# Performance work log

Measured on AMD Instinct MI355X. Metric: run time of the kernel, lower is better.

Reference implementation:

```python
import jax, jax.numpy as jnp
import numpy as np

N_NODES = 100000
N_EDGES = 1600000
HID = 64
EDGE_DIM = 16
SC_DIM = 6  # max_cycle(8) - MIN_CYCLE(3) + 1
N_LAYERS = 2
MSG_IN = 2 * HID + 2 * SC_DIM + EDGE_DIM  # 156
UPD_IN = 2 * HID


def setup_inputs() -> dict:
    key = jax.random.key(0)
    ks = jax.random.split(key, 16)
    s = 0.05
    inp = {
        "x": jax.random.normal(ks[0], (N_NODES, HID), dtype=jnp.float32),
        "edge_list": jax.random.randint(ks[1], (N_EDGES, 2), 0, N_NODES, dtype=jnp.int32),
        "node_struct": jax.random.randint(ks[2], (N_NODES, SC_DIM), 0, 4, dtype=jnp.int32),
        "edge_feature": jax.random.normal(ks[3], (N_EDGES, EDGE_DIM), dtype=jnp.float32),
        "edge_weight": jnp.ones((N_EDGES,), dtype=jnp.float32),
        "node2graph": jnp.sort(jax.random.randint(ks[4], (N_NODES,), 0, 128, dtype=jnp.int32)),
        "num_graphs": 128,
        # params
        "lin_w": jax.random.normal(ks[5], (HID, HID), dtype=jnp.float32) * s,
        "lin_b": jnp.zeros((HID,), dtype=jnp.float32),
        "msg_w1": jax.random.normal(ks[6], (N_LAYERS, MSG_IN, HID), dtype=jnp.float32) * s,
        "msg_b1": jnp.zeros((N_LAYERS, HID), dtype=jnp.float32),
        "msg_w2": jax.random.normal(ks[7], (N_LAYERS, HID, HID), dtype=jnp.float32) * s,
        "msg_b2": jnp.zeros((N_LAYERS, HID), dtype=jnp.float32),
        "upd_w1": jax.random.normal(ks[8], (N_LAYERS, UPD_IN, HID), dtype=jnp.float32) * s,
        "upd_b1": jnp.zeros((N_LAYERS, HID), dtype=jnp.float32),
        "upd_w2": jax.random.normal(ks[9], (N_LAYERS, HID, HID), dtype=jnp.float32) * s,
        "upd_b2": jnp.zeros((N_LAYERS, HID), dtype=jnp.float32),
    }
    return inp


def reference(x, edge_list, node_struct, edge_feature, edge_weight, node2graph,
              num_graphs, lin_w, lin_b, msg_w1, msg_b1, msg_w2, msg_b2,
              upd_w1, upd_b1, upd_w2, upd_b2):
    n_node = x.shape[0]
    src = edge_list[:, 0]
    dst = edge_list[:, 1]
    sc = node_struct.astype(x.dtype)          # [N, 6] structural cycle counts
    h = x @ lin_w + lin_b                      # input projection [N, HID]
    for l in range(N_LAYERS):
        # message: gather endpoints + structural feats + edge feats, 2-layer MLP
        m = jnp.concatenate([h[src], h[dst], sc[src], sc[dst], edge_feature], axis=-1)
        m = jax.nn.relu(m @ msg_w1[l] + msg_b1[l]) @ msg_w2[l] + msg_b2[l]
        # aggregate: weighted scatter_add onto destination nodes
        upd = jax.ops.segment_sum(m * edge_weight[:, None], dst, num_segments=n_node)
        # combine: cat(input, update) -> 2-layer MLP -> outer activation
        z = jnp.concatenate([h, upd], axis=-1)
        z = jax.nn.relu(z @ upd_w1[l] + upd_b1[l]) @ upd_w2[l] + upd_b2[l]
        h = jax.nn.relu(z)
    node_feature = h
    graph_feature = jax.ops.segment_sum(node_feature, node2graph, num_segments=num_graphs)
    return graph_feature, node_feature
```

## Files before the change

### kernel.cpp

```cpp
#include <hip/hip_runtime.h>

#define NN 100000
#define NE 1600000
#define HID 64
#define MSG_IN 156
#define W1E_OFF 140

__device__ __forceinline__ void mm4x4(float (&acc)[4][4], const float4 a, const float4 b) {
    acc[0][0] = fmaf(a.x, b.x, acc[0][0]);
    acc[0][1] = fmaf(a.x, b.y, acc[0][1]);
    acc[0][2] = fmaf(a.x, b.z, acc[0][2]);
    acc[0][3] = fmaf(a.x, b.w, acc[0][3]);
    acc[1][0] = fmaf(a.y, b.x, acc[1][0]);
    acc[1][1] = fmaf(a.y, b.y, acc[1][1]);
    acc[1][2] = fmaf(a.y, b.z, acc[1][2]);
    acc[1][3] = fmaf(a.y, b.w, acc[1][3]);
    acc[2][0] = fmaf(a.z, b.x, acc[2][0]);
    acc[2][1] = fmaf(a.z, b.y, acc[2][1]);
    acc[2][2] = fmaf(a.z, b.z, acc[2][2]);
    acc[2][3] = fmaf(a.z, b.w, acc[2][3]);
    acc[3][0] = fmaf(a.w, b.x, acc[3][0]);
    acc[3][1] = fmaf(a.w, b.y, acc[3][1]);
    acc[3][2] = fmaf(a.w, b.z, acc[3][2]);
    acc[3][3] = fmaf(a.w, b.w, acc[3][3]);
}


__global__ __launch_bounds__(256) void k_sw(
    const int2* __restrict__ el2, const float* __restrict__ ew,
    float* __restrict__ sw, int n_edges)
{
    int e = blockIdx.x * 256 + threadIdx.x;
    if (e < n_edges) atomicAdd(&sw[el2[e].y], ew[e]);
}

__global__ __launch_bounds__(256) void k_hist(
    const int2* __restrict__ el2, int* __restrict__ counts, int n_edges)
{
    int e = blockIdx.x * 256 + threadIdx.x;
    if (e < n_edges) atomicAdd(&counts[el2[e].y], 1);
}

__global__ __launch_bounds__(256) void k_scan1(
    const int* counts, int* offs, int* __restrict__ blksum, int n)
{
    __shared__ int s[256];
    const int tid = threadIdx.x;
    int i = blockIdx.x * 256 + tid;
    int v = (i < n) ? counts[i] : 0;
    s[tid] = v;
    for (int off = 1; off < 256; off <<= 1) {
        __syncthreads();
        int t = (tid >= off) ? s[tid - off] : 0;
        __syncthreads();
        s[tid] += t;
    }
    __syncthreads();
    if (i < n) offs[i] = s[tid] - v;
    if (tid == 255) blksum[blockIdx.x] = s[255];
}

__global__ __launch_bounds__(512) void k_scan2(int* __restrict__ blksum, int nb)
{
    __shared__ int s[512];
    const int tid = threadIdx.x;
    int v = (tid < nb) ? blksum[tid] : 0;
    s[tid] = v;
    for (int off = 1; off < 512; off <<= 1) {
        __syncthreads();
        int t = (tid >= off) ? s[tid - off] : 0;
        __syncthreads();
        s[tid] += t;
    }
    __syncthreads();
    if (tid < nb) blksum[tid] = s[tid] - v;
}

__global__ __launch_bounds__(256) void k_scan3(
    int* __restrict__ offs, const int* __restrict__ blksum, int n)
{
    int i = blockIdx.x * 256 + threadIdx.x;
    if (i < n) offs[i] += blksum[blockIdx.x];
}

__global__ __launch_bounds__(256) void k_permute(
    const int2* __restrict__ el2, int* __restrict__ cursor,
    int* __restrict__ perm, int n_edges)
{
    int e = blockIdx.x * 256 + threadIdx.x;
    if (e < n_edges) {
        int pos = atomicAdd(&cursor[el2[e].y], 1);
        perm[pos] = e;
    }
}

__global__ __launch_bounds__(256) void k_csmall(
    const float* __restrict__ msg_w2, const float* __restrict__ upd_w1,
    const float* __restrict__ msg_b2, float* __restrict__ C2, float* __restrict__ db2)
{
    const int l = blockIdx.x;
    const float* W2  = msg_w2 + (size_t)l * 4096;
    const float* U1b = upd_w1 + (size_t)l * 8192 + 4096;
    const float* b2  = msg_b2 + l * 64;
    float* C  = C2  + (size_t)l * 4096;
    float* db = db2 + l * 64;
    __shared__ __align__(16) float At[64][68];
    __shared__ __align__(16) float B[64][64];
    const int tid = threadIdx.x;
    for (int i = tid; i < 1024; i += 256) {
        ((float4*)B)[i] = ((const float4*)U1b)[i];
        int m = i >> 4, f4 = i & 15, k4 = f4 * 4;
        float4 v = ((const float4*)W2)[m * 16 + f4];
        At[k4 + 0][m] = v.x; At[k4 + 1][m] = v.y; At[k4 + 2][m] = v.z; At[k4 + 3][m] = v.w;
    }
    __syncthreads();
    const int ty = tid >> 4, tx = tid & 15;
    float acc[4][4];
    #pragma unroll
    for (int r = 0; r < 4; ++r) { acc[r][0]=0.f; acc[r][1]=0.f; acc[r][2]=0.f; acc[r][3]=0.f; }
    #pragma unroll 8
    for (int k = 0; k < 64; ++k) {
        float4 a = *(const float4*)&At[k][ty * 4];
        float4 bv = *(const float4*)&B[k][tx * 4];
        mm4x4(acc, a, bv);
    }
    #pragma unroll
    for (int r = 0; r < 4; ++r)
        ((float4*)C)[(ty * 4 + r) * 16 + tx] = make_float4(acc[r][0], acc[r][1], acc[r][2], acc[r][3]);
    if (tid < 64) {
        float sum = 0.f;
        for (int k = 0; k < 64; ++k) sum += b2[k] * B[k][tid];
        db[tid] = sum;
    }
}


__global__ __launch_bounds__(256) void k_init(
    const float* __restrict__ x, const float* __restrict__ w,
    const float* __restrict__ b, float* __restrict__ h, int n)
{
    __shared__ __align__(16) float At[64][68];
    __shared__ __align__(16) float B[64][64];
    const int tid = threadIdx.x;
    const int m0 = blockIdx.x * 64;
    for (int i = tid; i < 1024; i += 256)
        ((float4*)B)[i] = ((const float4*)w)[i];
    for (int i = tid; i < 1024; i += 256) {
        int m = i >> 4, f4 = i & 15, k4 = f4 * 4;
        int node = m0 + m;
        float4 v = make_float4(0.f, 0.f, 0.f, 0.f);
        if (node < n) v = ((const float4*)x)[node * 16 + f4];
        At[k4 + 0][m] = v.x; At[k4 + 1][m] = v.y; At[k4 + 2][m] = v.z; At[k4 + 3][m] = v.w;
    }
    __syncthreads();
    const int ty = tid >> 4, tx = tid & 15;
    float acc[4][4];
    {
        float4 bb = ((const float4*)b)[tx];
        #pragma unroll
        for (int r = 0; r < 4; ++r) { acc[r][0]=bb.x; acc[r][1]=bb.y; acc[r][2]=bb.z; acc[r][3]=bb.w; }
    }
    #pragma unroll 8
    for (int k = 0; k < 64; ++k) {
        float4 a = *(const float4*)&At[k][ty * 4];
        float4 bv = *(const float4*)&B[k][tx * 4];
        mm4x4(acc, a, bv);
    }
    #pragma unroll
    for (int r = 0; r < 4; ++r) {
        int node = m0 + ty * 4 + r;
        if (node < n)
            ((float4*)h)[node * 16 + tx] = make_float4(acc[r][0], acc[r][1], acc[r][2], acc[r][3]);
    }
}

__global__ __launch_bounds__(256) void k_pq(
    const float* __restrict__ h, const int* __restrict__ nsc,
    const float* __restrict__ w1, const float* __restrict__ b1,
    float* __restrict__ p, float* __restrict__ q, int n)
{
    __shared__ __align__(16) float At[64][68];
    __shared__ __align__(16) float Bp[64][64];
    __shared__ __align__(16) float Bq[64][64];
    __shared__ __align__(16) float Sct[6][68];
    __shared__ __align__(16) float Bc[6][64];
    __shared__ __align__(16) float Bd[6][64];
    const int tid = threadIdx.x;
    const int m0 = blockIdx.x * 64;
    for (int i = tid; i < 1024; i += 256) {
        ((float4*)Bp)[i] = ((const float4*)w1)[i];
        ((float4*)Bq)[i] = ((const float4*)(w1 + 64 * 64))[i];
    }
    if (tid < 96) {
        ((float4*)Bc)[tid] = ((const float4*)(w1 + 128 * 64))[tid];
        ((float4*)Bd)[tid] = ((const float4*)(w1 + 134 * 64))[tid];
    }
    for (int i = tid; i < 1024; i += 256) {
        int m = i >> 4, f4 = i & 15, k4 = f4 * 4;
        int node = m0 + m;
        float4 v = make_float4(0.f, 0.f, 0.f, 0.f);
        if (node < n) v = ((const float4*)h)[node * 16 + f4];
        At[k4 + 0][m] = v.x; At[k4 + 1][m] = v.y; At[k4 + 2][m] = v.z; At[k4 + 3][m] = v.w;
    }
    for (int i = tid; i < 384; i += 256) {
        int m = i & 63, k = i >> 6;
        int node = m0 + m;
        float v = 0.f;
        if (node < n) v = (float)nsc[node * 6 + k];
        Sct[k][m] = v;
    }
    __syncthreads();
    const int ty = tid >> 4, tx = tid & 15;
    float ap[4][4], aq[4][4];
    {
        float4 bb = ((const float4*)b1)[tx];
        #pragma unroll
        for (int r = 0; r < 4; ++r) {
            ap[r][0]=0.f; ap[r][1]=0.f; ap[r][2]=0.f; ap[r][3]=0.f;
            aq[r][0]=bb.x; aq[r][1]=bb.y; aq[r][2]=bb.z; aq[r][3]=bb.w;
        }
    }
    #pragma unroll 8
    for (int k = 0; k < 64; ++k) {
        float4 a  = *(const float4*)&At[k][ty * 4];
        float4 bp = *(const float4*)&Bp[k][tx * 4];
        float4 bq = *(const float4*)&Bq[k][tx * 4];
        mm4x4(ap, a, bp);
        mm4x4(aq, a, bq);
    }
    #pragma unroll
    for (int k = 0; k < 6; ++k) {
        float4 a  = *(const float4*)&Sct[k][ty * 4];
        float4 bc = *(const float4*)&Bc[k][tx * 4];
        float4 bd = *(const float4*)&Bd[k][tx * 4];
        mm4x4(ap, a, bc);
        mm4x4(aq, a, bd);
    }
    #pragma unroll
    for (int r = 0; r < 4; ++r) {
        int node = m0 + ty * 4 + r;
        if (node < n) {
            ((float4*)p)[node * 16 + tx] = make_float4(ap[r][0], ap[r][1], ap[r][2], ap[r][3]);
            ((float4*)q)[node * 16 + tx] = make_float4(aq[r][0], aq[r][1], aq[r][2], aq[r][3]);
        }
    }
}

__global__ __launch_bounds__(256) void k_edge_csr(
    const int* __restrict__ perm, const int* __restrict__ ends,
    const int2* __restrict__ el2,
    const float* __restrict__ ew, const float* __restrict__ ef,
    const float* __restrict__ p, const float* __restrict__ q,
    const float* __restrict__ w1e, float* __restrict__ S, int n_nodes)
{
    __shared__ __align__(16) float Et[16][68];
    __shared__ __align__(16) float W1e[16][64];
    __shared__ __align__(16) float Sacc[64][68];
    __shared__ int Ssrc[64];
    __shared__ int Sdst[64];
    __shared__ float Sew[64];
    const int tid = threadIdx.x;
    int b = blockIdx.x;
    {
        const int nb = gridDim.x;
        const int qn = nb >> 3, r = nb & 7;
        const int xcd = b & 7, idx = b >> 3;
        b = (xcd < r ? xcd * (qn + 1) : r * (qn + 1) + (xcd - r) * qn) + idx;
    }
    const int d0 = b * 64;
    const int dn = min(64, n_nodes - d0);
    const int eStart = (d0 == 0) ? 0 : ends[d0 - 1];
    const int eEnd   = ends[d0 + dn - 1];

    ((float4*)W1e)[tid] = ((const float4*)w1e)[tid];
    for (int i = tid; i < 64 * 17; i += 256)
        ((float4*)Sacc)[i] = make_float4(0.f, 0.f, 0.f, 0.f);

    const int ty = tid >> 4, tx = tid & 15;
    int curd = -1;
    float s0 = 0.f, s1 = 0.f, s2 = 0.f, s3 = 0.f;

    for (int c0 = eStart; c0 < eEnd; c0 += 64) {
        __syncthreads();
        if (tid < 64) {
            int e = c0 + tid;
            int s = 0, d = d0; float w = 0.f;
            if (e < eEnd) {
                int pe = perm[e];
                int2 sd = el2[pe];
                s = sd.x; d = sd.y; w = ew[pe];
            }
            Ssrc[tid] = s; Sdst[tid] = d; Sew[tid] = w;
        }
        {
            int e = tid >> 2, f4 = tid & 3, k4 = f4 * 4;
            int ge = c0 + e;
            float4 v = make_float4(0.f, 0.f, 0.f, 0.f);
            if (ge < eEnd) {
                int pe = perm[ge];
                v = ((const float4*)ef)[(size_t)pe * 4 + f4];
            }
            Et[k4 + 0][e] = v.x; Et[k4 + 1][e] = v.y; Et[k4 + 2][e] = v.z; Et[k4 + 3][e] = v.w;
        }
        __syncthreads();
        float acc[4][4];
        #pragma unroll
        for (int r = 0; r < 4; ++r) {
            int s = Ssrc[ty * 4 + r], d = Sdst[ty * 4 + r];
            float4 pv = ((const float4*)p)[(size_t)s * 16 + tx];
            float4 qv = ((const float4*)q)[(size_t)d * 16 + tx];
            acc[r][0] = pv.x + qv.x; acc[r][1] = pv.y + qv.y;
            acc[r][2] = pv.z + qv.z; acc[r][3] = pv.w + qv.w;
        }
        #pragma unroll
        for (int k = 0; k < 16; ++k) {
            float4 a = *(const float4*)&Et[k][ty * 4];
            float4 bv = *(const float4*)&W1e[k][tx * 4];
            mm4x4(acc, a, bv);
        }
        #pragma unroll
        for (int r = 0; r < 4; ++r) {
            int le = ty * 4 + r;
            int ge = c0 + le;
            if (ge < eEnd) {
                int d = Sdst[le];
                float w = Sew[le];
                float v0 = fmaxf(acc[r][0], 0.f) * w;
                float v1 = fmaxf(acc[r][1], 0.f) * w;
                float v2 = fmaxf(acc[r][2], 0.f) * w;
                float v3 = fmaxf(acc[r][3], 0.f) * w;
                if (d != curd) {
                    if (curd >= 0) {
                        float* dp = &Sacc[curd - d0][tx * 4];
                        atomicAdd(dp + 0, s0); atomicAdd(dp + 1, s1);
                        atomicAdd(dp + 2, s2); atomicAdd(dp + 3, s3);
                    }
                    curd = d; s0 = v0; s1 = v1; s2 = v2; s3 = v3;
                } else {
                    s0 += v0; s1 += v1; s2 += v2; s3 += v3;
                }
            }
        }
    }
    if (curd >= 0) {
        float* dp = &Sacc[curd - d0][tx * 4];
        atomicAdd(dp + 0, s0); atomicAdd(dp + 1, s1);
        atomicAdd(dp + 2, s2); atomicAdd(dp + 3, s3);
    }
    __syncthreads();
    for (int i = tid; i < dn * 16; i += 256) {
        int row = i >> 4, f4 = i & 15;
        ((float4*)S)[(size_t)(d0 + row) * 16 + f4] = *(const float4*)&Sacc[row][f4 * 4];
    }
}

__global__ __launch_bounds__(256) void k_edge2(
    const int* __restrict__ perm, const int2* __restrict__ el2,
    const float* __restrict__ ew, const float* __restrict__ ef,
    const float* __restrict__ p, const float* __restrict__ q,
    const float* __restrict__ w1e, float* __restrict__ S, int n_edges)
{
    __shared__ __align__(16) float Et[16][68];
    __shared__ __align__(16) float W1e[16][64];
    __shared__ int Ssrc[64];
    __shared__ int Sdst[64];
    __shared__ float Sew[64];
    const int tid = threadIdx.x;
    const int b = blockIdx.x, nb = gridDim.x;
    const int tile = ((nb & 7) == 0) ? ((b & 7) * (nb >> 3) + (b >> 3)) : b;
    const int e0 = tile * 64;
    if (tid < 64) {
        int e = e0 + tid;
        int s = 0, d = 0; float w = 0.f;
        if (e < n_edges) {
            int pe = perm ? perm[e] : e;
            int2 sd = el2[pe];
            s = sd.x; d = sd.y; w = ew[pe];
        }
        Ssrc[tid] = s; Sdst[tid] = d; Sew[tid] = w;
    }
    ((float4*)W1e)[tid] = ((const float4*)w1e)[tid];
    {
        int e = tid >> 2, f4 = tid & 3, k4 = f4 * 4;
        int ge = e0 + e;
        float4 v = make_float4(0.f, 0.f, 0.f, 0.f);
        if (ge < n_edges) {
            int pe = perm ? perm[ge] : ge;
            v = ((const float4*)ef)[(size_t)pe * 4 + f4];
        }
        Et[k4 + 0][e] = v.x; Et[k4 + 1][e] = v.y; Et[k4 + 2][e] = v.z; Et[k4 + 3][e] = v.w;
    }
    __syncthreads();
    const int ty = tid >> 4, tx = tid & 15;
    float acc[4][4];
    #pragma unroll
    for (int r = 0; r < 4; ++r) {
        int s = Ssrc[ty * 4 + r], d = Sdst[ty * 4 + r];
        float4 pv = ((const float4*)p)[(size_t)s * 16 + tx];
        float4 qv = ((const float4*)q)[(size_t)d * 16 + tx];
        acc[r][0] = pv.x + qv.x; acc[r][1] = pv.y + qv.y;
        acc[r][2] = pv.z + qv.z; acc[r][3] = pv.w + qv.w;
    }
    #pragma unroll
    for (int k = 0; k < 16; ++k) {
        float4 a = *(const float4*)&Et[k][ty * 4];
        float4 bv = *(const float4*)&W1e[k][tx * 4];
        mm4x4(acc, a, bv);
    }
    {
        int curd = -1;
        float s0 = 0.f, s1 = 0.f, s2 = 0.f, s3 = 0.f;
        #pragma unroll
        for (int r = 0; r < 4; ++r) {
            int le = ty * 4 + r;
            int ge = e0 + le;
            if (ge < n_edges) {
                int d = Sdst[le];
                float w = Sew[le];
                float v0 = fmaxf(acc[r][0], 0.f) * w;
                float v1 = fmaxf(acc[r][1], 0.f) * w;
                float v2 = fmaxf(acc[r][2], 0.f) * w;
                float v3 = fmaxf(acc[r][3], 0.f) * w;
                if (d != curd) {
                    if (curd >= 0) {
                        atomicAdd(&S[(size_t)curd * 64 + tx * 4 + 0], s0);
                        atomicAdd(&S[(size_t)curd * 64 + tx * 4 + 1], s1);
                        atomicAdd(&S[(size_t)curd * 64 + tx * 4 + 2], s2);
                        atomicAdd(&S[(size_t)curd * 64 + tx * 4 + 3], s3);
                    }
                    curd = d; s0 = v0; s1 = v1; s2 = v2; s3 = v3;
                } else {
                    s0 += v0; s1 += v1; s2 += v2; s3 += v3;
                }
            }
        }
        if (curd >= 0) {
            atomicAdd(&S[(size_t)curd * 64 + tx * 4 + 0], s0);
            atomicAdd(&S[(size_t)curd * 64 + tx * 4 + 1], s1);
            atomicAdd(&S[(size_t)curd * 64 + tx * 4 + 2], s2);
            atomicAdd(&S[(size_t)curd * 64 + tx * 4 + 3], s3);
        }
    }
}

__global__ __launch_bounds__(256) void k_update(
    float* __restrict__ h, const float* __restrict__ S,
    const float* __restrict__ w1, const float* __restrict__ C,
    const float* __restrict__ b1, const float* __restrict__ w2,
    const float* __restrict__ b2, const float* __restrict__ db,
    const float* __restrict__ sw,
    int n, int write_out, float* __restrict__ out_graph,
    const int* __restrict__ n2g)
{
    __shared__ __align__(16) float At[64][68];
    __shared__ __align__(16) float B1[128][64];
    __shared__ float Db[64];
    const int tid = threadIdx.x;
    const int m0 = blockIdx.x * 64;
    const int ty = tid >> 4, tx = tid & 15;
    if (tid < 64) Db[tid] = db[tid];
    for (int i = tid; i < 2048; i += 256)
        ((float4*)B1)[i] = (i < 1024) ? ((const float4*)w1)[i] : ((const float4*)C)[i - 1024];
    for (int i = tid; i < 1024; i += 256) {
        int m = i >> 4, f4 = i & 15, k4 = f4 * 4;
        int node = m0 + m;
        float4 v = make_float4(0.f, 0.f, 0.f, 0.f);
        if (node < n) v = ((const float4*)h)[node * 16 + f4];
        At[k4 + 0][m] = v.x; At[k4 + 1][m] = v.y; At[k4 + 2][m] = v.z; At[k4 + 3][m] = v.w;
    }
    __syncthreads();
    float acc[4][4];
    {
        float4 bb = ((const float4*)b1)[tx];
        #pragma unroll
        for (int r = 0; r < 4; ++r) { acc[r][0]=bb.x; acc[r][1]=bb.y; acc[r][2]=bb.z; acc[r][3]=bb.w; }
    }
    #pragma unroll 8
    for (int k = 0; k < 64; ++k) {
        float4 a = *(const float4*)&At[k][ty * 4];
        float4 bv = *(const float4*)&B1[k][tx * 4];
        mm4x4(acc, a, bv);
    }
    __syncthreads();
    for (int i = tid; i < 1024; i += 256) {
        int m = i >> 4, f4 = i & 15, k4 = f4 * 4;
        int node = m0 + m;
        float4 v = make_float4(0.f, 0.f, 0.f, 0.f);
        if (node < n) v = ((const float4*)S)[node * 16 + f4];
        At[k4 + 0][m] = v.x; At[k4 + 1][m] = v.y; At[k4 + 2][m] = v.z; At[k4 + 3][m] = v.w;
    }
    __syncthreads();
    #pragma unroll 8
    for (int k = 0; k < 64; ++k) {
        float4 a = *(const float4*)&At[k][ty * 4];
        float4 bv = *(const float4*)&B1[64 + k][tx * 4];
        mm4x4(acc, a, bv);
    }
    #pragma unroll
    for (int r = 0; r < 4; ++r) {
        int node = m0 + ty * 4 + r;
        float swv = (node < n) ? sw[node] : 0.f;
        #pragma unroll
        for (int c = 0; c < 4; ++c)
            acc[r][c] = fmaf(swv, Db[tx * 4 + c], acc[r][c]);
    }
    __syncthreads();
    #pragma unroll
    for (int r = 0; r < 4; ++r)
        #pragma unroll
        for (int c = 0; c < 4; ++c)
            At[tx * 4 + c][ty * 4 + r] = fmaxf(acc[r][c], 0.f);
    for (int i = tid; i < 1024; i += 256)
        ((float4*)B1)[i] = ((const float4*)w2)[i];
    __syncthreads();
    float acc2[4][4];
    {
        float4 bb = ((const float4*)b2)[tx];
        #pragma unroll
        for (int r = 0; r < 4; ++r) { acc2[r][0]=bb.x; acc2[r][1]=bb.y; acc2[r][2]=bb.z; acc2[r][3]=bb.w; }
    }
    #pragma unroll 8
    for (int k = 0; k < 64; ++k) {
        float4 a = *(const float4*)&At[k][ty * 4];
        float4 bv = *(const float4*)&B1[k][tx * 4];
        mm4x4(acc2, a, bv);
    }
    float hv[4][4];
    #pragma unroll
    for (int r = 0; r < 4; ++r)
        #pragma unroll
        for (int c = 0; c < 4; ++c)
            hv[r][c] = fmaxf(acc2[r][c], 0.f);
    #pragma unroll
    for (int r = 0; r < 4; ++r) {
        int node = m0 + ty * 4 + r;
        if (node < n)
            ((float4*)h)[node * 16 + tx] = make_float4(hv[r][0], hv[r][1], hv[r][2], hv[r][3]);
    }
    if (write_out) {
        int curg = -1;
        float s0 = 0.f, s1 = 0.f, s2 = 0.f, s3 = 0.f;
        #pragma unroll
        for (int r = 0; r < 4; ++r) {
            int node = m0 + ty * 4 + r;
            if (node < n) {
                int g = n2g[node];
                if (g != curg) {
                    if (curg >= 0) {
                        atomicAdd(&out_graph[curg * 64 + tx * 4 + 0], s0);
                        atomicAdd(&out_graph[curg * 64 + tx * 4 + 1], s1);
                        atomicAdd(&out_graph[curg * 64 + tx * 4 + 2], s2);
                        atomicAdd(&out_graph[curg * 64 + tx * 4 + 3], s3);
                    }
                    curg = g; s0 = hv[r][0]; s1 = hv[r][1]; s2 = hv[r][2]; s3 = hv[r][3];
                } else {
                    s0 += hv[r][0]; s1 += hv[r][1]; s2 += hv[r][2]; s3 += hv[r][3];
                }
            }
        }
        if (curg >= 0) {
            atomicAdd(&out_graph[curg * 64 + tx * 4 + 0], s0);
            atomicAdd(&out_graph[curg * 64 + tx * 4 + 1], s1);
            atomicAdd(&out_graph[curg * 64 + tx * 4 + 2], s2);
            atomicAdd(&out_graph[curg * 64 + tx * 4 + 3], s3);
        }
    }
}

extern "C" void kernel_launch(void* const* d_in, const int* in_sizes, int n_in,
                              void* d_out, int out_size, void* d_ws, size_t ws_size,
                              hipStream_t stream)
{
    const float* x       = (const float*)d_in[0];
    const int2*  el2     = (const int2*)d_in[1];
    const int*   nsc     = (const int*)d_in[2];
    const float* ef      = (const float*)d_in[3];
    const float* ew      = (const float*)d_in[4];
    const int*   n2g     = (const int*)d_in[5];
    const float* lin_w   = (const float*)d_in[7];
    const float* lin_b   = (const float*)d_in[8];
    const float* msg_w1  = (const float*)d_in[9];
    const float* msg_b1  = (const float*)d_in[10];
    const float* msg_w2  = (const float*)d_in[11];
    const float* upd_w1  = (const float*)d_in[13];
    const float* upd_b1  = (const float*)d_in[14];
    const float* upd_w2  = (const float*)d_in[15];
    const float* upd_b2  = (const float*)d_in[16];
    const float* msg_b2  = (const float*)d_in[12];

    float* out_graph = (float*)d_out;
    float* h   = (float*)d_out + 128 * 64;

    const size_t NNH = (size_t)NN * HID;
    float* p  = (float*)d_ws;
    float* q  = p + NNH;
    float* S  = q + NNH;
    char*  cur = (char*)(S + NNH);
    const size_t base   = 3 * NNH * sizeof(float);
    const size_t szPerm = (size_t)NE * sizeof(int);
    const size_t szCnt  = (size_t)NN * sizeof(int);
    const size_t szSw   = (size_t)NN * sizeof(float);
    const size_t szBlk  = 4096;
    const size_t szC    = 2 * 64 * 64 * sizeof(float);
    const size_t szDb   = 2 * 64 * sizeof(float);
    const size_t need_sort = base + szPerm + szCnt + szBlk + szSw + szC + szDb;

    int *perm = nullptr, *counts = nullptr, *blksum = nullptr;
    float *sw, *C2, *db2;
    const int do_sort = (ws_size >= need_sort) ? 1 : 0;
    if (do_sort) {
        perm   = (int*)cur;        cur += szPerm;
        counts = (int*)cur;        cur += szCnt;
        blksum = (int*)cur;        cur += szBlk;
    }
    sw  = (float*)cur;             cur += szSw;
    C2  = (float*)cur;             cur += szC;
    db2 = (float*)cur;

    const int nblk_n  = (NN + 63) / 64;
    const int nblk_e  = (NE + 63) / 64;
    const int nblk_eh = (NE + 255) / 256;
    const int nblk_sc = (NN + 255) / 256;

    hipMemsetAsync(d_out, 0, 128 * 64 * sizeof(float), stream);
    hipMemsetAsync(sw, 0, szSw, stream);
    k_sw<<<nblk_eh, 256, 0, stream>>>(el2, ew, sw, NE);

    if (do_sort) {
        hipMemsetAsync(counts, 0, szCnt, stream);
        k_hist<<<nblk_eh, 256, 0, stream>>>(el2, counts, NE);
        k_scan1<<<nblk_sc, 256, 0, stream>>>(counts, counts, blksum, NN);
        k_scan2<<<1, 512, 0, stream>>>(blksum, nblk_sc);
        k_scan3<<<nblk_sc, 256, 0, stream>>>(counts, blksum, NN);
        k_permute<<<nblk_eh, 256, 0, stream>>>(el2, counts, perm, NE);
    }
    k_csmall<<<2, 256, 0, stream>>>(msg_w2, upd_w1, msg_b2, C2, db2);

    k_init<<<nblk_n, 256, 0, stream>>>(x, lin_w, lin_b, h, NN);
    for (int l = 0; l < 2; ++l) {
        const float* w1 = msg_w1 + (size_t)l * MSG_IN * HID;
        k_pq<<<nblk_n, 256, 0, stream>>>(h, nsc, w1, msg_b1 + l * HID, p, q, NN);
        if (do_sort) {
            k_edge_csr<<<nblk_n, 256, 0, stream>>>(perm, counts, el2, ew, ef, p, q,
                                                   w1 + W1E_OFF * HID, S, NN);
        } else {
            hipMemsetAsync(S, 0, NNH * sizeof(float), stream);
            k_edge2<<<nblk_e, 256, 0, stream>>>(nullptr, el2, ew, ef, p, q,
                                                w1 + W1E_OFF * HID, S, NE);
        }
        k_update<<<nblk_n, 256, 0, stream>>>(h, S,
                                             upd_w1 + (size_t)l * 2 * HID * HID,
                                             C2 + (size_t)l * 4096,
                                             upd_b1 + l * HID,
                                             upd_w2 + (size_t)l * HID * HID,
                                             upd_b2 + l * HID,
                                             db2 + l * 64, sw,
                                             NN, (l == 1) ? 1 : 0, out_graph, n2g);
    }
}
```

Measured before the change: 1.336 ms.

## Bucket edges by destination block and source range to localize gathers

Edges are now sorted by a composite key of destination 64-node block and source bucket (2048 nodes) instead of by exact destination. Within each destination block, gathers of source features then fall in nearby address ranges, which is meant to improve cache locality. The cost is that the per-destination run merge in the edge kernel is gone, so every edge now issues LDS atomics. The edge-weight sum is also folded into the histogram kernel to save one pass over the edge list.

Result: slower. 2.084 ms (+56.0%).

```diff
diff --git a/kernel.cpp b/kernel.cpp
--- a/kernel.cpp
+++ b/kernel.cpp
@@ -5,6 +5,9 @@
 #define HID 64
 #define MSG_IN 156
 #define W1E_OFF 140
+#define NBLK_D 1563
+#define NSB 49
+#define KEYS (NBLK_D * NSB)
 
 __device__ __forceinline__ void mm4x4(float (&acc)[4][4], const float4 a, const float4 b) {
     acc[0][0] = fmaf(a.x, b.x, acc[0][0]);
@@ -34,11 +37,16 @@
     if (e < n_edges) atomicAdd(&sw[el2[e].y], ew[e]);
 }
 
-__global__ __launch_bounds__(256) void k_hist(
-    const int2* __restrict__ el2, int* __restrict__ counts, int n_edges)
+__global__ __launch_bounds__(256) void k_hist2(
+    const int2* __restrict__ el2, const float* __restrict__ ew,
+    int* __restrict__ counts, float* __restrict__ sw, int n_edges)
 {
     int e = blockIdx.x * 256 + threadIdx.x;
-    if (e < n_edges) atomicAdd(&counts[el2[e].y], 1);
+    if (e < n_edges) {
+        int2 sd = el2[e];
+        atomicAdd(&counts[(sd.y >> 6) * NSB + (sd.x >> 11)], 1);
+        atomicAdd(&sw[sd.y], ew[e]);
+    }
 }
 
 __global__ __launch_bounds__(256) void k_scan1(
@@ -83,13 +91,15 @@
     if (i < n) offs[i] += blksum[blockIdx.x];
 }
 
-__global__ __launch_bounds__(256) void k_permute(
+__global__ __launch_bounds__(256) void k_permute2(
     const int2* __restrict__ el2, int* __restrict__ cursor,
     int* __restrict__ perm, int n_edges)
 {
     int e = blockIdx.x * 256 + threadIdx.x;
     if (e < n_edges) {
-        int pos = atomicAdd(&cursor[el2[e].y], 1);
+        int2 sd = el2[e];
+        int key = (sd.y >> 6) * NSB + (sd.x >> 11);
+        int pos = atomicAdd(&cursor[key], 1);
         perm[pos] = e;
     }
 }
@@ -247,7 +257,7 @@
 }
 
 __global__ __launch_bounds__(256) void k_edge_csr(
-    const int* __restrict__ perm, const int* __restrict__ ends,
+    const int* __restrict__ perm, const int* __restrict__ kends,
     const int2* __restrict__ el2,
     const float* __restrict__ ew, const float* __restrict__ ef,
     const float* __restrict__ p, const float* __restrict__ q,
@@ -263,22 +273,21 @@
     int b = blockIdx.x;
     {
         const int nb = gridDim.x;
-        const int qn = nb >> 3, r = nb & 7;
+        const int qn = nb >> 3, rr = nb & 7;
         const int xcd = b & 7, idx = b >> 3;
-        b = (xcd < r ? xcd * (qn + 1) : r * (qn + 1) + (xcd - r) * qn) + idx;
+        b = (xcd < rr ? xcd * (qn + 1) : rr * (qn + 1) + (xcd - rr) * qn) + idx;
     }
     const int d0 = b * 64;
     const int dn = min(64, n_nodes - d0);
-    const int eStart = (d0 == 0) ? 0 : ends[d0 - 1];
-    const int eEnd   = ends[d0 + dn - 1];
+    const int kbase = b * NSB;
+    const int eStart = (b == 0) ? 0 : kends[kbase - 1];
+    const int eEnd   = kends[kbase + NSB - 1];
 
     ((float4*)W1e)[tid] = ((const float4*)w1e)[tid];
     for (int i = tid; i < 64 * 17; i += 256)
         ((float4*)Sacc)[i] = make_float4(0.f, 0.f, 0.f, 0.f);
 
     const int ty = tid >> 4, tx = tid & 15;
-    int curd = -1;
-    float s0 = 0.f, s1 = 0.f, s2 = 0.f, s3 = 0.f;
 
     for (int c0 = eStart; c0 < eEnd; c0 += 64) {
         __syncthreads();
@@ -321,31 +330,16 @@
         #pragma unroll
         for (int r = 0; r < 4; ++r) {
             int le = ty * 4 + r;
-            int ge = c0 + le;
-            if (ge < eEnd) {
+            if (c0 + le < eEnd) {
                 int d = Sdst[le];
                 float w = Sew[le];
-                float v0 = fmaxf(acc[r][0], 0.f) * w;
-                float v1 = fmaxf(acc[r][1], 0.f) * w;
-                float v2 = fmaxf(acc[r][2], 0.f) * w;
-                float v3 = fmaxf(acc[r][3], 0.f) * w;
-                if (d != curd) {
-                    if (curd >= 0) {
-                        float* dp = &Sacc[curd - d0][tx * 4];
-                        atomicAdd(dp + 0, s0); atomicAdd(dp + 1, s1);
-                        atomicAdd(dp + 2, s2); atomicAdd(dp + 3, s3);
-                    }
-                    curd = d; s0 = v0; s1 = v1; s2 = v2; s3 = v3;
-                } else {
-                    s0 += v0; s1 += v1; s2 += v2; s3 += v3;
-                }
+                float* dp = &Sacc[d - d0][tx * 4];
+                atomicAdd(dp + 0, fmaxf(acc[r][0], 0.f) * w);
+                atomicAdd(dp + 1, fmaxf(acc[r][1], 0.f) * w);
+                atomicAdd(dp + 2, fmaxf(acc[r][2], 0.f) * w);
+                atomicAdd(dp + 3, fmaxf(acc[r][3], 0.f) * w);
             }
         }
-    }
-    if (curd >= 0) {
-        float* dp = &Sacc[curd - d0][tx * 4];
-        atomicAdd(dp + 0, s0); atomicAdd(dp + 1, s1);
-        atomicAdd(dp + 2, s2); atomicAdd(dp + 3, s3);
     }
     __syncthreads();
     for (int i = tid; i < dn * 16; i += 256) {
@@ -620,19 +614,20 @@
     const int nblk_n  = (NN + 63) / 64;
     const int nblk_e  = (NE + 63) / 64;
     const int nblk_eh = (NE + 255) / 256;
-    const int nblk_sc = (NN + 255) / 256;
+    const int nblk_k  = (KEYS + 255) / 256;
 
     hipMemsetAsync(d_out, 0, 128 * 64 * sizeof(float), stream);
     hipMemsetAsync(sw, 0, szSw, stream);
-    k_sw<<<nblk_eh, 256, 0, stream>>>(el2, ew, sw, NE);
 
     if (do_sort) {
         hipMemsetAsync(counts, 0, szCnt, stream);
-        k_hist<<<nblk_eh, 256, 0, stream>>>(el2, counts, NE);
-        k_scan1<<<nblk_sc, 256, 0, stream>>>(counts, counts, blksum, NN);
-        k_scan2<<<1, 512, 0, stream>>>(blksum, nblk_sc);
-        k_scan3<<<nblk_sc, 256, 0, stream>>>(counts, blksum, NN);
-        k_permute<<<nblk_eh, 256, 0, stream>>>(el2, counts, perm, NE);
+        k_hist2<<<nblk_eh, 256, 0, stream>>>(el2, ew, counts, sw, NE);
+        k_scan1<<<nblk_k, 256, 0, stream>>>(counts, counts, blksum, KEYS);
+        k_scan2<<<1, 512, 0, stream>>>(blksum, nblk_k);
+        k_scan3<<<nblk_k, 256, 0, stream>>>(counts, blksum, KEYS);
+        k_permute2<<<nblk_eh, 256, 0, stream>>>(el2, counts, perm, NE);
+    } else {
+        k_sw<<<nblk_eh, 256, 0, stream>>>(el2, ew, sw, NE);
     }
     k_csmall<<<2, 256, 0, stream>>>(msg_w2, upd_w1, msg_b2, C2, db2);
 
```
